# Optimization experiments

Hardware: AMD Instinct MI355X
Metric: run time of the kernel (lower is better)

Reference implementation:

```python
import jax, jax.numpy as jnp
import numpy as np
from jax import lax

VOCAB, EMBED, HIDDEN, SEQ = 50257, 1024, 1024, 4096


def setup_inputs() -> dict:
    key = jax.random.key(0)
    ks = jax.random.split(key, 8)
    s = 0.02
    return {
        "input_seq": jax.random.randint(ks[0], (SEQ,), 0, VOCAB),
        "emb": jax.random.normal(ks[1], (VOCAB, EMBED), jnp.float32) * s,
        "Wrx": jax.random.normal(ks[2], (HIDDEN, EMBED), jnp.float32) * s,
        "Wrh": jax.random.normal(ks[3], (HIDDEN, HIDDEN), jnp.float32) * s,
        "Wzx": jax.random.normal(ks[4], (HIDDEN, EMBED), jnp.float32) * s,
        "Wzh": jax.random.normal(ks[5], (HIDDEN, HIDDEN), jnp.float32) * s,
        "Wx": jax.random.normal(ks[6], (HIDDEN, EMBED), jnp.float32) * s,
        "Wh": jax.random.normal(ks[7], (HIDDEN, HIDDEN), jnp.float32) * s,
    }


def reference(input_seq, emb, Wrx, Wrh, Wzx, Wzh, Wx, Wh):
    # Embed whole sequence at once: [S, E]
    x_seq = emb[input_seq]
    # Hoist input-side projections out of the recurrence (one GEMM each): [S, H]
    xr = x_seq @ Wrx.T
    xz = x_seq @ Wzx.T
    xh = x_seq @ Wx.T

    def step(h, xs):
        xr_t, xz_t, xh_t = xs
        z = jax.nn.sigmoid(xz_t + Wzh @ h)          # update gate
        r = jax.nn.sigmoid(xr_t + Wrh @ h)          # reset gate
        h_tilde = jnp.tanh(xh_t + Wh @ (r * h))     # candidate
        h_new = z * h + (1.0 - z) * h_tilde
        return h_new, None

    h0 = jnp.zeros((Wh.shape[0],), dtype=emb.dtype)
    h_final, _ = lax.scan(step, h0, (xr, xz, xh))
    return h_final
```

## Files before the change

kernel.cpp:

```cpp
#include <hip/hip_runtime.h>
#include <stdint.h>


#define HID    1024
#define SEQLEN 4096
#define NWG    128
#define RPW    8
#define BLOCK  256

typedef unsigned long long u64;

__global__ __launch_bounds__(BLOCK) void proj_gemm(
    const int* __restrict__ seq, const float* __restrict__ emb,
    const float* __restrict__ Wrx, const float* __restrict__ Wzx,
    const float* __restrict__ Wx,
    float* __restrict__ xr, float* __restrict__ xz, float* __restrict__ xh)
{
  __shared__ float As[32][68];
  __shared__ float Bs[32][68];
  __shared__ int   idx[64];

  const float* W = (blockIdx.z == 0) ? Wrx : (blockIdx.z == 1) ? Wzx : Wx;
  float*       C = (blockIdx.z == 0) ? xr  : (blockIdx.z == 1) ? xz  : xh;

  const int tid = threadIdx.x;
  const int t0 = blockIdx.y * 64;
  const int i0 = blockIdx.x * 64;
  if (tid < 64) idx[tid] = seq[t0 + tid];
  __syncthreads();

  float acc[4][4] = {};
  const int tx = tid & 15, ty = tid >> 4;
  const int c4 = (tid & 7) * 4;
  const int r8 = tid >> 3;

  for (int k0 = 0; k0 < HID; k0 += 32) {
    for (int l = 0; l < 2; ++l) {
      const int rr = r8 + l * 32;
      float4 av = *(const float4*)(emb + (size_t)idx[rr] * HID + k0 + c4);
      As[c4+0][rr]=av.x; As[c4+1][rr]=av.y; As[c4+2][rr]=av.z; As[c4+3][rr]=av.w;
      float4 bv = *(const float4*)(W + (size_t)(i0 + rr) * HID + k0 + c4);
      Bs[c4+0][rr]=bv.x; Bs[c4+1][rr]=bv.y; Bs[c4+2][rr]=bv.z; Bs[c4+3][rr]=bv.w;
    }
    __syncthreads();
    #pragma unroll
    for (int k = 0; k < 32; ++k) {
      float a[4], b[4];
      *(float4*)a = *(const float4*)&As[k][ty * 4];
      *(float4*)b = *(const float4*)&Bs[k][tx * 4];
      #pragma unroll
      for (int i = 0; i < 4; ++i)
        #pragma unroll
        for (int j = 0; j < 4; ++j)
          acc[i][j] = fmaf(a[i], b[j], acc[i][j]);
    }
    __syncthreads();
  }
  #pragma unroll
  for (int i = 0; i < 4; ++i) {
    float4 v = make_float4(acc[i][0], acc[i][1], acc[i][2], acc[i][3]);
    *(float4*)(C + (size_t)(t0 + ty * 4 + i) * HID + i0 + tx * 4) = v;
  }
}

__device__ __forceinline__ void load2_f4_coherent(const float* p0, const float* p1,
                                                  float4* a, float4* b) {
  float4 va, vb;
  asm volatile("global_load_dwordx4 %0, %2, off sc0 sc1\n\t"
               "global_load_dwordx4 %1, %3, off sc0 sc1\n\t"
               "s_waitcnt vmcnt(0)"
               : "=&v"(va), "=&v"(vb) : "v"(p0), "v"(p1) : "memory");
  *a = va; *b = vb;
}

__device__ __forceinline__ void publish2(u64* cells, int row, float a, float b,
                                         unsigned tag) {
  u64 ca = ((u64)tag << 32) | (u64)__float_as_uint(a);
  u64 cb = ((u64)tag << 32) | (u64)__float_as_uint(b);
  __hip_atomic_store(&cells[row],     ca, __ATOMIC_RELAXED, __HIP_MEMORY_SCOPE_AGENT);
  __hip_atomic_store(&cells[row + 1], cb, __ATOMIC_RELAXED, __HIP_MEMORY_SCOPE_AGENT);
}

__device__ __forceinline__ void exchange_read(const u64* cells, unsigned want,
                                              float* dst_lds, int wave, int lane,
                                              int* budget) {
  const int c0 = wave * 256 + 2 * lane;
  const int c1 = c0 + 128;
  const float* p0 = (const float*)(cells + c0);
  const float* p1 = (const float*)(cells + c1);
  float4 v0, v1;
  for (;;) {
    load2_f4_coherent(p0, p1, &v0, &v1);
    if (__float_as_uint(v0.y) == want && __float_as_uint(v0.w) == want &&
        __float_as_uint(v1.y) == want && __float_as_uint(v1.w) == want) break;
    if (--(*budget) <= 0) break;
  }
  *(float2*)&dst_lds[c0] = make_float2(v0.x, v0.z);
  *(float2*)&dst_lds[c1] = make_float2(v1.x, v1.z);
}

__global__ __launch_bounds__(BLOCK, 1) void rnn_scan(
    const float* __restrict__ Wzh, const float* __restrict__ Wrh,
    const float* __restrict__ Whh,
    const float* __restrict__ xz, const float* __restrict__ xr,
    const float* __restrict__ xh,
    u64* __restrict__ hcell,
    u64* __restrict__ rhcell,
    float* __restrict__ out)
{
  const int tid  = threadIdx.x;
  const int wave = tid >> 6, lane = tid & 63;
  const int g    = blockIdx.x;
  const int rowA = g * RPW + wave * 2;

  __shared__ float h_lds[HID];
  __shared__ float rh_lds[HID];

  float wgt[3][2][16];
  #pragma unroll
  for (int m = 0; m < 3; ++m) {
    const float* Wm = (m == 0) ? Wzh : (m == 1) ? Wrh : Whh;
    #pragma unroll
    for (int rr = 0; rr < 2; ++rr) {
      const float* p = Wm + (size_t)(rowA + rr) * HID + lane * 4;
      #pragma unroll
      for (int q = 0; q < 4; ++q) {
        float4 v = *(const float4*)(p + q * 256);
        wgt[m][rr][q*4+0] = v.x; wgt[m][rr][q*4+1] = v.y;
        wgt[m][rr][q*4+2] = v.z; wgt[m][rr][q*4+3] = v.w;
      }
    }
  }

  int budget = 1 << 22;
  float xzv[2], xrv[2], xhv[2], zv[2], hprev[2];

  for (int t = 1; t <= SEQLEN; ++t) {
    if (lane == 0) {
      #pragma unroll
      for (int rr = 0; rr < 2; ++rr) {
        xzv[rr] = xz[(size_t)(t - 1) * HID + rowA + rr];
        xrv[rr] = xr[(size_t)(t - 1) * HID + rowA + rr];
        xhv[rr] = xh[(size_t)(t - 1) * HID + rowA + rr];
      }
    }

    if (t == 1) {
      const int c0 = wave * 256 + 2 * lane, c1 = c0 + 128;
      *(float2*)&h_lds[c0] = make_float2(0.f, 0.f);
      *(float2*)&h_lds[c1] = make_float2(0.f, 0.f);
    } else {
      exchange_read(hcell + ((t - 1) & 1) * HID, (unsigned)(t - 1),
                    h_lds, wave, lane, &budget);
    }
    __syncthreads();

    float hr[16];
    #pragma unroll
    for (int q = 0; q < 4; ++q)
      *(float4*)&hr[q*4] = *(const float4*)&h_lds[q * 256 + lane * 4];
    float az[2] = {0.f, 0.f}, ar[2] = {0.f, 0.f};
    #pragma unroll
    for (int rr = 0; rr < 2; ++rr)
      #pragma unroll
      for (int c = 0; c < 16; ++c) {
        az[rr] = fmaf(wgt[0][rr][c], hr[c], az[rr]);
        ar[rr] = fmaf(wgt[1][rr][c], hr[c], ar[rr]);
      }
    #pragma unroll
    for (int m = 1; m < 64; m <<= 1) {
      az[0] += __shfl_xor(az[0], m, 64);
      az[1] += __shfl_xor(az[1], m, 64);
      ar[0] += __shfl_xor(ar[0], m, 64);
      ar[1] += __shfl_xor(ar[1], m, 64);
    }
    if (lane == 0) {
      float rh[2];
      #pragma unroll
      for (int rr = 0; rr < 2; ++rr) {
        hprev[rr] = h_lds[rowA + rr];
        zv[rr]    = 1.f / (1.f + __expf(-(xzv[rr] + az[rr])));
        float rg  = 1.f / (1.f + __expf(-(xrv[rr] + ar[rr])));
        rh[rr]    = rg * hprev[rr];
      }
      publish2(rhcell + (t & 1) * HID, rowA, rh[0], rh[1], (unsigned)t);
    }

    exchange_read(rhcell + (t & 1) * HID, (unsigned)t, rh_lds, wave, lane, &budget);
    __syncthreads();

    float rr16[16];
    #pragma unroll
    for (int q = 0; q < 4; ++q)
      *(float4*)&rr16[q*4] = *(const float4*)&rh_lds[q * 256 + lane * 4];
    float ac[2] = {0.f, 0.f};
    #pragma unroll
    for (int rr = 0; rr < 2; ++rr)
      #pragma unroll
      for (int c = 0; c < 16; ++c)
        ac[rr] = fmaf(wgt[2][rr][c], rr16[c], ac[rr]);
    #pragma unroll
    for (int m = 1; m < 64; m <<= 1) {
      ac[0] += __shfl_xor(ac[0], m, 64);
      ac[1] += __shfl_xor(ac[1], m, 64);
    }
    if (lane == 0) {
      float hn[2];
      #pragma unroll
      for (int rr = 0; rr < 2; ++rr) {
        float cand = tanhf(xhv[rr] + ac[rr]);
        hn[rr]     = zv[rr] * hprev[rr] + (1.f - zv[rr]) * cand;
      }
      publish2(hcell + (t & 1) * HID, rowA, hn[0], hn[1], (unsigned)t);
      if (t == SEQLEN) { out[rowA] = hn[0]; out[rowA + 1] = hn[1]; }
    }
  }
}

extern "C" void kernel_launch(void* const* d_in, const int* in_sizes, int n_in,
                              void* d_out, int out_size, void* d_ws, size_t ws_size,
                              hipStream_t stream) {
  (void)in_sizes; (void)n_in; (void)out_size; (void)ws_size;

  const int*   seq = (const int*)d_in[0];
  const float* emb = (const float*)d_in[1];
  const float* Wrx = (const float*)d_in[2];
  const float* Wrh = (const float*)d_in[3];
  const float* Wzx = (const float*)d_in[4];
  const float* Wzh = (const float*)d_in[5];
  const float* Wx  = (const float*)d_in[6];
  const float* Wh  = (const float*)d_in[7];

  char* ws = (char*)d_ws;
  const size_t PROJ = (size_t)SEQLEN * HID * sizeof(float);
  float* xr    = (float*)(ws);
  float* xz    = (float*)(ws + PROJ);
  float* xh    = (float*)(ws + 2 * PROJ);
  u64*   hcell = (u64*)(ws + 3 * PROJ);
  u64*   rhcell= hcell + 2 * HID;

  (void)hipMemsetAsync(hcell, 0xFF, 4 * HID * sizeof(u64), stream);

  proj_gemm<<<dim3(HID / 64, SEQLEN / 64, 3), BLOCK, 0, stream>>>(
      seq, emb, Wrx, Wzx, Wx, xr, xz, xh);

  rnn_scan<<<dim3(NWG), BLOCK, 0, stream>>>(
      Wzh, Wrh, Wh, xz, xr, xh, hcell, rhcell, (float*)d_out);
}
```

Baseline: 24.63 ms.

## Halve scan workgroups to 64 with 512 threads, poll one pair per thread

Cuts the persistent recurrence grid from 128 to 64 workgroups of 512 threads, each workgroup still owning 2 rows per wave (16 rows total). Each thread now polls a single 16-byte pair of tagged cells instead of two, so the exchange of h and r*h is spread over more threads with fewer global loads per thread. Fewer workgroups mean fewer participants in the per-step cross-workgroup exchange, which is meant to reduce contention and the polling latency that gates each timestep. The trade-off is larger blocks, whose __syncthreads covers 8 waves, plus a changed launch bound and a halved spin budget.

```diff
diff --git a/kernel.cpp b/kernel.cpp
--- a/kernel.cpp
+++ b/kernel.cpp
@@ -4,13 +4,13 @@
 
 #define HID    1024
 #define SEQLEN 4096
-#define NWG    128
-#define RPW    8
-#define BLOCK  256
+#define NWG    64
+#define RPW    16
+#define BLOCK  512
 
 typedef unsigned long long u64;
 
-__global__ __launch_bounds__(BLOCK) void proj_gemm(
+__global__ __launch_bounds__(256) void proj_gemm(
     const int* __restrict__ seq, const float* __restrict__ emb,
     const float* __restrict__ Wrx, const float* __restrict__ Wzx,
     const float* __restrict__ Wx,
@@ -63,16 +63,6 @@
   }
 }
 
-__device__ __forceinline__ void load2_f4_coherent(const float* p0, const float* p1,
-                                                  float4* a, float4* b) {
-  float4 va, vb;
-  asm volatile("global_load_dwordx4 %0, %2, off sc0 sc1\n\t"
-               "global_load_dwordx4 %1, %3, off sc0 sc1\n\t"
-               "s_waitcnt vmcnt(0)"
-               : "=&v"(va), "=&v"(vb) : "v"(p0), "v"(p1) : "memory");
-  *a = va; *b = vb;
-}
-
 __device__ __forceinline__ void publish2(u64* cells, int row, float a, float b,
                                          unsigned tag) {
   u64 ca = ((u64)tag << 32) | (u64)__float_as_uint(a);
@@ -81,25 +71,20 @@
   __hip_atomic_store(&cells[row + 1], cb, __ATOMIC_RELAXED, __HIP_MEMORY_SCOPE_AGENT);
 }
 
-__device__ __forceinline__ void exchange_read(const u64* cells, unsigned want,
-                                              float* dst_lds, int wave, int lane,
-                                              int* budget) {
-  const int c0 = wave * 256 + 2 * lane;
-  const int c1 = c0 + 128;
-  const float* p0 = (const float*)(cells + c0);
-  const float* p1 = (const float*)(cells + c1);
-  float4 v0, v1;
+__device__ __forceinline__ float2 poll_pair(const u64* cells, int pair,
+                                            unsigned want, int* budget) {
+  const float* p = (const float*)(cells + 2 * pair);
+  float4 v;
   for (;;) {
-    load2_f4_coherent(p0, p1, &v0, &v1);
-    if (__float_as_uint(v0.y) == want && __float_as_uint(v0.w) == want &&
-        __float_as_uint(v1.y) == want && __float_as_uint(v1.w) == want) break;
+    asm volatile("global_load_dwordx4 %0, %1, off sc0 sc1\n\ts_waitcnt vmcnt(0)"
+                 : "=v"(v) : "v"(p) : "memory");
+    if (__float_as_uint(v.y) == want && __float_as_uint(v.w) == want) break;
     if (--(*budget) <= 0) break;
   }
-  *(float2*)&dst_lds[c0] = make_float2(v0.x, v0.z);
-  *(float2*)&dst_lds[c1] = make_float2(v1.x, v1.z);
-}
-
-__global__ __launch_bounds__(BLOCK, 1) void rnn_scan(
+  return make_float2(v.x, v.z);
+}
+
+__global__ __launch_bounds__(BLOCK, 2) void rnn_scan(
     const float* __restrict__ Wzh, const float* __restrict__ Wrh,
     const float* __restrict__ Whh,
     const float* __restrict__ xz, const float* __restrict__ xr,
@@ -132,10 +117,18 @@
     }
   }
 
-  int budget = 1 << 22;
+  int budget = 1 << 21;
   float xzv[2], xrv[2], xhv[2], zv[2], hprev[2];
 
   for (int t = 1; t <= SEQLEN; ++t) {
+    if (t == 1) {
+      *(float2*)&h_lds[2 * tid] = make_float2(0.f, 0.f);
+    } else {
+      float2 hv = poll_pair(hcell + ((t - 1) & 1) * HID, tid,
+                            (unsigned)(t - 1), &budget);
+      *(float2*)&h_lds[2 * tid] = hv;
+    }
+
     if (lane == 0) {
       #pragma unroll
       for (int rr = 0; rr < 2; ++rr) {
@@ -143,15 +136,6 @@
         xrv[rr] = xr[(size_t)(t - 1) * HID + rowA + rr];
         xhv[rr] = xh[(size_t)(t - 1) * HID + rowA + rr];
       }
-    }
-
-    if (t == 1) {
-      const int c0 = wave * 256 + 2 * lane, c1 = c0 + 128;
-      *(float2*)&h_lds[c0] = make_float2(0.f, 0.f);
-      *(float2*)&h_lds[c1] = make_float2(0.f, 0.f);
-    } else {
-      exchange_read(hcell + ((t - 1) & 1) * HID, (unsigned)(t - 1),
-                    h_lds, wave, lane, &budget);
     }
     __syncthreads();
 
@@ -186,7 +170,10 @@
       publish2(rhcell + (t & 1) * HID, rowA, rh[0], rh[1], (unsigned)t);
     }
 
-    exchange_read(rhcell + (t & 1) * HID, (unsigned)t, rh_lds, wave, lane, &budget);
+    {
+      float2 rv = poll_pair(rhcell + (t & 1) * HID, tid, (unsigned)t, &budget);
+      *(float2*)&rh_lds[2 * tid] = rv;
+    }
     __syncthreads();
 
     float rr16[16];
@@ -241,7 +228,7 @@
 
   (void)hipMemsetAsync(hcell, 0xFF, 4 * HID * sizeof(u64), stream);
 
-  proj_gemm<<<dim3(HID / 64, SEQLEN / 64, 3), BLOCK, 0, stream>>>(
+  proj_gemm<<<dim3(HID / 64, SEQLEN / 64, 3), 256, 0, stream>>>(
       seq, emb, Wrx, Wzx, Wx, xr, xz, xh);
 
   rnn_scan<<<dim3(NWG), BLOCK, 0, stream>>>(
```

Result: faster. 24.05 ms (-2.3%).
